# Kernel optimization log

Hardware: AMD Instinct MI355X
Metric: run time of the kernel (lower is better)

Reference implementation:

```python
import jax, jax.numpy as jnp
import numpy as np

EPS = 1e-5  # torch BatchNorm1d default

def _silu(x):
    return x * jax.nn.sigmoid(x)

def _bn(x, g, b, rm, rv, axis):
    # eval-mode batchnorm along given channel axis
    shape = [1] * x.ndim
    shape[axis] = -1
    return (x - rm.reshape(shape)) * (g.reshape(shape) / jnp.sqrt(rv.reshape(shape) + EPS)) + b.reshape(shape)

def setup_inputs() -> dict:
    key = jax.random.key(0)
    ks = jax.random.split(key, 12)
    b, n, p, d, r = 64, 256, 12, 128, 2
    x = jax.random.normal(ks[0], (b, n, p, d), dtype=jnp.float32)
    # k branch: Conv1d(p -> 1, k=1, bias=False) + BN(1)
    wk = jax.random.normal(ks[1], (p,), dtype=jnp.float32) / np.sqrt(p)
    bn_k_g = jax.random.uniform(ks[2], (1,), dtype=jnp.float32, minval=0.5, maxval=1.5)
    bn_k_b = 0.1 * jax.random.normal(ks[3], (1,), dtype=jnp.float32)
    bn_k_rm = jnp.zeros((1,), jnp.float32)
    bn_k_rv = jnp.ones((1,), jnp.float32)
    # v branch: Conv1d(d -> d, k=1, bias=False) + BN(d)
    wv = jax.random.normal(ks[4], (d, d), dtype=jnp.float32) / np.sqrt(d)
    bn_v_g = jax.random.uniform(ks[5], (d,), dtype=jnp.float32, minval=0.5, maxval=1.5)
    bn_v_b = 0.1 * jax.random.normal(ks[6], (d,), dtype=jnp.float32)
    bn_v_rm = jnp.zeros((d,), jnp.float32)
    bn_v_rv = jnp.ones((d,), jnp.float32)
    # fc_avg / fc_max: Linear(n, n//r, bias=False) -> GELU -> Linear(n//r, n, bias=False)
    w_avg1 = jax.random.normal(ks[7], (n // r, n), dtype=jnp.float32) / np.sqrt(n)
    w_avg2 = jax.random.normal(ks[8], (n, n // r), dtype=jnp.float32) / np.sqrt(n // r)
    w_max1 = jax.random.normal(ks[9], (n // r, n), dtype=jnp.float32) / np.sqrt(n)
    w_max2 = jax.random.normal(ks[10], (n, n // r), dtype=jnp.float32) / np.sqrt(n // r)
    return dict(x=x, wk=wk, bn_k_g=bn_k_g, bn_k_b=bn_k_b, bn_k_rm=bn_k_rm, bn_k_rv=bn_k_rv,
                wv=wv, bn_v_g=bn_v_g, bn_v_b=bn_v_b, bn_v_rm=bn_v_rm, bn_v_rv=bn_v_rv,
                w_avg1=w_avg1, w_avg2=w_avg2, w_max1=w_max1, w_max2=w_max2)

def _forward(x, wk, bn_k_g, bn_k_b, bn_k_rm, bn_k_rv, wv, bn_v_g, bn_v_b, bn_v_rm, bn_v_rv,
             w_avg1, w_avg2, w_max1, w_max2):
    b, n, p, d = x.shape
    xf = x.reshape(b * n, p, d)
    # squeeze-excite gates: pool over d, FC over n
    avg = jnp.mean(xf, axis=-1).reshape(b, n, p).transpose(0, 2, 1)  # [b,p,n]
    mx = jnp.max(xf, axis=-1).reshape(b, n, p).transpose(0, 2, 1)    # [b,p,n]
    gelu = lambda t: jax.nn.gelu(t, approximate=False)
    avg_g = jax.nn.sigmoid(gelu(avg @ w_avg1.T) @ w_avg2.T).transpose(0, 2, 1)  # [b,n,p]
    max_g = jax.nn.sigmoid(gelu(mx @ w_max1.T) @ w_max2.T).transpose(0, 2, 1)   # [b,n,p]
    # k: 1x1 conv over p channels -> [bn, d], BN(1ch), SiLU, softmax over d
    k_raw = jnp.einsum('bpd,p->bd', xf, wk)
    k = jax.nn.softmax(_silu(k_raw * (bn_k_g / jnp.sqrt(bn_k_rv + EPS)) - bn_k_rm * (bn_k_g / jnp.sqrt(bn_k_rv + EPS)) + bn_k_b), axis=-1)  # [bn,d]
    # v: 1x1 conv over d channels on [bn,d,p], BN(d), SiLU -> [bn,p,d]
    v_raw = jnp.einsum('bpd,ed->bpe', xf, wv)  # channel axis is last here
    v = _silu(_bn(v_raw, bn_v_g, bn_v_b, bn_v_rm, bn_v_rv, axis=2))  # [bn,p,d]
    # y = v @ k : [bn,p];  y_pool = (max+avg) @ v : [bn,d]
    y = jnp.einsum('bpd,bd->bp', v, k)
    pool = (max_g + avg_g).reshape(b * n, p)
    y_pool = jnp.einsum('bp,bpd->bd', pool, v)
    out = y_pool[:, None, :] * y[:, :, None]  # [bn,p,d]
    return out.reshape(b, n, p, d)

def reference(x, wk, bn_k_g, bn_k_b, bn_k_rm, bn_k_rv, wv, bn_v_g, bn_v_b, bn_v_rm, bn_v_rv,
              w_avg1, w_avg2, w_max1, w_max2):
    return _forward(x, wk, bn_k_g, bn_k_b, bn_k_rm, bn_k_rv, wv, bn_v_g, bn_v_b, bn_v_rm, bn_v_rv,
                    w_avg1, w_avg2, w_max1, w_max2)
```

## Files before the change

kernel.cpp:

```cpp
#include <hip/hip_runtime.h>
#include <hip/hip_bf16.h>

#define B_   64
#define N_   256
#define P_   12
#define D_   128
#define BN_  (B_*N_)
#define EPSV 1e-5f

typedef float  f32x4  __attribute__((ext_vector_type(4)));
typedef __bf16 bf16x8 __attribute__((ext_vector_type(8)));
typedef __bf16 bf16x4 __attribute__((ext_vector_type(4)));

__device__ float g_avg[768*256];
__device__ float g_mx [768*256];
__device__ float g_h1 [1536*128];
__device__ float g_pool[BN_*P_];

__device__ inline float sigm_(float x) { return 1.0f / (1.0f + __expf(-x)); }

__device__ inline float dot4_(float4 a, float4 b, float acc) {
  acc = fmaf(a.x, b.x, acc); acc = fmaf(a.y, b.y, acc);
  acc = fmaf(a.z, b.z, acc); acc = fmaf(a.w, b.w, acc);
  return acc;
}

__global__ __launch_bounds__(256) void k1_pool(const float* __restrict__ x) {
  int w = threadIdx.x >> 6, l = threadIdx.x & 63;
  int bn = blockIdx.x * 4 + w;
  const float* xp = x + (size_t)bn * (P_ * D_);
  int b = bn >> 8, n = bn & 255;
  float sacc[P_], macc[P_];
#pragma unroll
  for (int p = 0; p < P_; ++p) {
    float2 v = *(const float2*)(xp + p * D_ + 2 * l);
    float s = v.x + v.y;
    float m = fmaxf(v.x, v.y);
#pragma unroll
    for (int off = 32; off; off >>= 1) {
      s += __shfl_xor(s, off);
      m = fmaxf(m, __shfl_xor(m, off));
    }
    sacc[p] = s * (1.0f / D_);
    macc[p] = m;
  }
  if (l == 0) {
#pragma unroll
    for (int p = 0; p < P_; ++p) {
      g_avg[(b * P_ + p) * N_ + n] = sacc[p];
      g_mx [(b * P_ + p) * N_ + n] = macc[p];
    }
  }
}

__global__ __launch_bounds__(256) void k2_l1(const float* __restrict__ w_avg1,
                                             const float* __restrict__ w_max1) {
  __shared__ float in_t[16 * 256];
  __shared__ float w_t[64 * 68];
  int t = threadIdx.x;
  int rblk = blockIdx.x % 96, cblk = blockIdx.x / 96;
  int rr0 = rblk * 16, c0 = cblk * 64;
  bool mxb = (rr0 >= 768);
  int r768 = mxb ? rr0 - 768 : rr0;
  const float* in = (mxb ? g_mx : g_avg) + (size_t)r768 * 256;
  const float* w1 = mxb ? w_max1 : w_avg1;
#pragma unroll
  for (int i = 0; i < 4; ++i) {
    int F = t + i * 256, r = F >> 6, k4 = F & 63;
    *(float4*)(in_t + r * 256 + k4 * 4) = *(const float4*)(in + r * 256 + k4 * 4);
  }
  int c = t & 63, rq = t >> 6;
  float a0 = 0, a1 = 0, a2 = 0, a3 = 0;
  for (int kc = 0; kc < 4; ++kc) {
    __syncthreads();
#pragma unroll
    for (int i = 0; i < 4; ++i) {
      int F = t + i * 256, cr = F >> 4, k4 = F & 15;
      *(float4*)(w_t + cr * 68 + k4 * 4) =
          *(const float4*)(w1 + (size_t)(c0 + cr) * 256 + kc * 64 + k4 * 4);
    }
    __syncthreads();
#pragma unroll
    for (int k4 = 0; k4 < 16; ++k4) {
      float4 wv4 = *(float4*)(w_t + c * 68 + k4 * 4);
      a0 = dot4_(*(float4*)(in_t + (rq * 4 + 0) * 256 + kc * 64 + k4 * 4), wv4, a0);
      a1 = dot4_(*(float4*)(in_t + (rq * 4 + 1) * 256 + kc * 64 + k4 * 4), wv4, a1);
      a2 = dot4_(*(float4*)(in_t + (rq * 4 + 2) * 256 + kc * 64 + k4 * 4), wv4, a2);
      a3 = dot4_(*(float4*)(in_t + (rq * 4 + 3) * 256 + kc * 64 + k4 * 4), wv4, a3);
    }
  }
  float accs[4] = {a0, a1, a2, a3};
#pragma unroll
  for (int r = 0; r < 4; ++r) {
    float a = accs[r];
    float g = 0.5f * a * (1.0f + erff(a * 0.70710678f));
    g_h1[(size_t)(rr0 + rq * 4 + r) * 128 + c0 + c] = g;
  }
}

__global__ __launch_bounds__(256) void k2_l2(const float* __restrict__ w_avg2,
                                             const float* __restrict__ w_max2) {
  __shared__ float ina_t[16 * 128];
  __shared__ float inm_t[16 * 128];
  __shared__ float wa_t[64 * 68];
  __shared__ float wm_t[64 * 68];
  int t = threadIdx.x;
  int rblk = blockIdx.x % 48, cblk = blockIdx.x / 48;
  int rr0 = rblk * 16, n0 = cblk * 64;
#pragma unroll
  for (int i = 0; i < 2; ++i) {
    int F = t + i * 256, r = F >> 5, k4 = F & 31;
    *(float4*)(ina_t + r * 128 + k4 * 4) = *(const float4*)(g_h1 + (size_t)(rr0 + r) * 128 + k4 * 4);
    *(float4*)(inm_t + r * 128 + k4 * 4) = *(const float4*)(g_h1 + (size_t)(768 + rr0 + r) * 128 + k4 * 4);
  }
  int c = t & 63, rq = t >> 6;
  float aa0=0, aa1=0, aa2=0, aa3=0, am0=0, am1=0, am2=0, am3=0;
  for (int kc = 0; kc < 2; ++kc) {
    __syncthreads();
#pragma unroll
    for (int i = 0; i < 4; ++i) {
      int F = t + i * 256, cr = F >> 4, k4 = F & 15;
      *(float4*)(wa_t + cr * 68 + k4 * 4) =
          *(const float4*)(w_avg2 + (size_t)(n0 + cr) * 128 + kc * 64 + k4 * 4);
      *(float4*)(wm_t + cr * 68 + k4 * 4) =
          *(const float4*)(w_max2 + (size_t)(n0 + cr) * 128 + kc * 64 + k4 * 4);
    }
    __syncthreads();
#pragma unroll
    for (int k4 = 0; k4 < 16; ++k4) {
      float4 wa4 = *(float4*)(wa_t + c * 68 + k4 * 4);
      float4 wm4 = *(float4*)(wm_t + c * 68 + k4 * 4);
      float4 i0 = *(float4*)(ina_t + (rq * 4 + 0) * 128 + kc * 64 + k4 * 4);
      float4 i1 = *(float4*)(ina_t + (rq * 4 + 1) * 128 + kc * 64 + k4 * 4);
      float4 i2 = *(float4*)(ina_t + (rq * 4 + 2) * 128 + kc * 64 + k4 * 4);
      float4 i3 = *(float4*)(ina_t + (rq * 4 + 3) * 128 + kc * 64 + k4 * 4);
      aa0 = dot4_(i0, wa4, aa0); aa1 = dot4_(i1, wa4, aa1);
      aa2 = dot4_(i2, wa4, aa2); aa3 = dot4_(i3, wa4, aa3);
      float4 j0 = *(float4*)(inm_t + (rq * 4 + 0) * 128 + kc * 64 + k4 * 4);
      float4 j1 = *(float4*)(inm_t + (rq * 4 + 1) * 128 + kc * 64 + k4 * 4);
      float4 j2 = *(float4*)(inm_t + (rq * 4 + 2) * 128 + kc * 64 + k4 * 4);
      float4 j3 = *(float4*)(inm_t + (rq * 4 + 3) * 128 + kc * 64 + k4 * 4);
      am0 = dot4_(j0, wm4, am0); am1 = dot4_(j1, wm4, am1);
      am2 = dot4_(j2, wm4, am2); am3 = dot4_(j3, wm4, am3);
    }
  }
  float va[4] = {aa0, aa1, aa2, aa3};
  float vm[4] = {am0, am1, am2, am3};
#pragma unroll
  for (int r = 0; r < 4; ++r) {
    int rr = rr0 + rq * 4 + r;
    int b = rr / 12, p = rr % 12;
    float pv = sigm_(va[r]) + sigm_(vm[r]);
    g_pool[((size_t)b * 256 + (n0 + c)) * 12 + p] = pv;
  }
}

__global__ __launch_bounds__(256) void k3_main(
    const float* __restrict__ x,  const float* __restrict__ wk,
    const float* __restrict__ kg, const float* __restrict__ kb,
    const float* __restrict__ krm, const float* __restrict__ krv,
    const float* __restrict__ wv,
    const float* __restrict__ vg, const float* __restrict__ vb,
    const float* __restrict__ vrm, const float* __restrict__ vrv,
    float* __restrict__ out) {
  __shared__ __align__(16) __bf16 wv_lds[128 * 128];
  __shared__ float sv_l[128], tv_l[128];
  __shared__ float v_l[4][12 * 128];

  int t = threadIdx.x, w = t >> 6, l = t & 63;
  if (t < 128) {
    float s = vg[t] * rsqrtf(vrv[t] + EPSV);
    sv_l[t] = s;
    tv_l[t] = vb[t] - vrm[t] * s;
  }
  __syncthreads();
  {
    int e = t >> 1, dh = (t & 1) * 64;
    float s = sv_l[e];
    int swz = (e & 7) << 4;
#pragma unroll
    for (int i = 0; i < 16; ++i) {
      float4 v4 = *(const float4*)(wv + (size_t)e * 128 + dh + i * 4);
      bf16x4 h;
      h[0] = (__bf16)(v4.x * s); h[1] = (__bf16)(v4.y * s);
      h[2] = (__bf16)(v4.z * s); h[3] = (__bf16)(v4.w * s);
      int byte = (e * 256 + (dh + i * 4) * 2) ^ swz;
      *(bf16x4*)((char*)wv_lds + byte) = h;
    }
  }
  float ksc = kg[0] * rsqrtf(krv[0] + EPSV);
  float kbs = kb[0] - krm[0] * ksc;
  __syncthreads();

  int arow = (l & 15) > 11 ? 11 : (l & 15);
  int ak = (l >> 4) * 8;
  int bcol = l & 15;
  int bko = (l >> 4) * 16;

  for (int it = 0; it < 4; ++it) {
    int bn = blockIdx.x * 16 + it * 4 + w;
    const float* xp = x + (size_t)bn * (P_ * D_);

    bf16x8 afr[4];
#pragma unroll
    for (int ks = 0; ks < 4; ++ks) {
      const float* src = xp + arow * 128 + ks * 32 + ak;
      float4 lo = *(const float4*)(src);
      float4 hi = *(const float4*)(src + 4);
      bf16x8 a;
      a[0] = (__bf16)lo.x; a[1] = (__bf16)lo.y; a[2] = (__bf16)lo.z; a[3] = (__bf16)lo.w;
      a[4] = (__bf16)hi.x; a[5] = (__bf16)hi.y; a[6] = (__bf16)hi.z; a[7] = (__bf16)hi.w;
      afr[ks] = a;
    }

    float kr0 = 0, kr1 = 0;
#pragma unroll
    for (int p = 0; p < P_; ++p) {
      float2 xv = *(const float2*)(xp + p * 128 + 2 * l);
      float wkp = wk[p];
      kr0 = fmaf(xv.x, wkp, kr0);
      kr1 = fmaf(xv.y, wkp, kr1);
    }
    float z0 = kr0 * ksc + kbs, z1 = kr1 * ksc + kbs;
    z0 = z0 * sigm_(z0);
    z1 = z1 * sigm_(z1);
    float mmax = fmaxf(z0, z1);
#pragma unroll
    for (int off = 32; off; off >>= 1) mmax = fmaxf(mmax, __shfl_xor(mmax, off));
    float e0 = __expf(z0 - mmax), e1 = __expf(z1 - mmax);
    float es = e0 + e1;
#pragma unroll
    for (int off = 32; off; off >>= 1) es += __shfl_xor(es, off);
    float inv = 1.0f / es;
    float k0 = e0 * inv, k1 = e1 * inv;

    f32x4 acc[8];
#pragma unroll
    for (int nt = 0; nt < 8; ++nt) acc[nt] = (f32x4){0.f, 0.f, 0.f, 0.f};
#pragma unroll
    for (int nt = 0; nt < 8; ++nt) {
      int er = bcol + nt * 16;
      int base = er * 256;
      int sw = (er & 7) << 4;
#pragma unroll
      for (int ks = 0; ks < 4; ++ks) {
        int byte = (base + ks * 64 + bko) ^ sw;
        bf16x8 bfr = *(const bf16x8*)((const char*)wv_lds + byte);
        acc[nt] = __builtin_amdgcn_mfma_f32_16x16x32_bf16(afr[ks], bfr, acc[nt], 0, 0, 0);
      }
    }

    int p0 = (l >> 4) * 4;
    if (p0 < 12) {
#pragma unroll
      for (int nt = 0; nt < 8; ++nt) {
        int e = bcol + nt * 16;
        float tvv = tv_l[e];
#pragma unroll
        for (int r = 0; r < 4; ++r) {
          float a = acc[nt][r] + tvv;
          float v = a * sigm_(a);
          v_l[w][(p0 + r) * 128 + e] = v;
        }
      }
    }
    __syncthreads();

    const float* pp = g_pool + (size_t)bn * 12;
    float pl[P_];
#pragma unroll
    for (int p = 0; p < P_; ++p) pl[p] = pp[p];
    float yp0 = 0, yp1 = 0;
    float ypart[P_];
#pragma unroll
    for (int p = 0; p < P_; ++p) {
      float2 vvp = *(const float2*)(&v_l[w][0] + p * 128 + 2 * l);
      ypart[p] = vvp.x * k0 + vvp.y * k1;
      yp0 = fmaf(pl[p], vvp.x, yp0);
      yp1 = fmaf(pl[p], vvp.y, yp1);
    }
#pragma unroll
    for (int p = 0; p < P_; ++p) {
      float s = ypart[p];
#pragma unroll
      for (int off = 32; off; off >>= 1) s += __shfl_xor(s, off);
      ypart[p] = s;
    }
    float* op = out + (size_t)bn * (P_ * D_);
#pragma unroll
    for (int p = 0; p < P_; ++p) {
      float2 o;
      o.x = yp0 * ypart[p];
      o.y = yp1 * ypart[p];
      *(float2*)(op + p * 128 + 2 * l) = o;
    }
    __syncthreads();
  }
}

extern "C" void kernel_launch(void* const* d_in, const int* in_sizes, int n_in,
                              void* d_out, int out_size, void* d_ws, size_t ws_size,
                              hipStream_t stream) {
  const float* x   = (const float*)d_in[0];
  const float* wk  = (const float*)d_in[1];
  const float* kg  = (const float*)d_in[2];
  const float* kbb = (const float*)d_in[3];
  const float* krm = (const float*)d_in[4];
  const float* krv = (const float*)d_in[5];
  const float* wvp = (const float*)d_in[6];
  const float* vg  = (const float*)d_in[7];
  const float* vbb = (const float*)d_in[8];
  const float* vrm = (const float*)d_in[9];
  const float* vrv = (const float*)d_in[10];
  const float* wa1 = (const float*)d_in[11];
  const float* wa2 = (const float*)d_in[12];
  const float* wm1 = (const float*)d_in[13];
  const float* wm2 = (const float*)d_in[14];
  float* out = (float*)d_out;

  k1_pool<<<4096, 256, 0, stream>>>(x);
  k2_l1<<<192, 256, 0, stream>>>(wa1, wm1);
  k2_l2<<<192, 256, 0, stream>>>(wa2, wm2);
  k3_main<<<1024, 256, 0, stream>>>(x, wk, kg, kbb, krm, krv, wvp, vg, vbb, vrm, vrv, out);
}
```

Before: 123.1 us.

## Drop block barriers in main loop, pad V tile, widen pool loads

Each wavefront in the main kernel works on its own private v_l slice, so the two __syncthreads per iteration are removed and the wave relies on in-wave ordering instead. The v_l row stride is padded to 130 floats to cut LDS bank conflicts, and the g_pool gate loads are moved ahead of the MFMA section so their latency overlaps compute. The pooling kernel now uses float4 loads with two p rows per wave (32-lane reductions). Removing the barriers assumes LDS writes and reads within one wavefront are ordered without an explicit wave barrier, which is a correctness risk.

```diff
diff --git a/kernel.cpp b/kernel.cpp
--- a/kernel.cpp
+++ b/kernel.cpp
@@ -7,6 +7,7 @@
 #define D_   128
 #define BN_  (B_*N_)
 #define EPSV 1e-5f
+#define VST  130
 
 typedef float  f32x4  __attribute__((ext_vector_type(4)));
 typedef __bf16 bf16x8 __attribute__((ext_vector_type(8)));
@@ -29,26 +30,29 @@
   int w = threadIdx.x >> 6, l = threadIdx.x & 63;
   int bn = blockIdx.x * 4 + w;
   const float* xp = x + (size_t)bn * (P_ * D_);
-  int b = bn >> 8, n = bn & 255;
-  float sacc[P_], macc[P_];
-#pragma unroll
-  for (int p = 0; p < P_; ++p) {
-    float2 v = *(const float2*)(xp + p * D_ + 2 * l);
-    float s = v.x + v.y;
-    float m = fmaxf(v.x, v.y);
-#pragma unroll
-    for (int off = 32; off; off >>= 1) {
+  int half = l >> 5, lane32 = l & 31;
+  float s6[6], m6[6];
+#pragma unroll
+  for (int pp = 0; pp < 6; ++pp) {
+    int p = pp * 2 + half;
+    float4 v = *(const float4*)(xp + p * D_ + lane32 * 4);
+    float s = (v.x + v.y) + (v.z + v.w);
+    float m = fmaxf(fmaxf(v.x, v.y), fmaxf(v.z, v.w));
+#pragma unroll
+    for (int off = 16; off; off >>= 1) {
       s += __shfl_xor(s, off);
       m = fmaxf(m, __shfl_xor(m, off));
     }
-    sacc[p] = s * (1.0f / D_);
-    macc[p] = m;
-  }
-  if (l == 0) {
-#pragma unroll
-    for (int p = 0; p < P_; ++p) {
-      g_avg[(b * P_ + p) * N_ + n] = sacc[p];
-      g_mx [(b * P_ + p) * N_ + n] = macc[p];
+    s6[pp] = s * (1.0f / D_);
+    m6[pp] = m;
+  }
+  if (lane32 == 0) {
+    int b = bn >> 8, n = bn & 255;
+#pragma unroll
+    for (int pp = 0; pp < 6; ++pp) {
+      int p = pp * 2 + half;
+      g_avg[(b * P_ + p) * N_ + n] = s6[pp];
+      g_mx [(b * P_ + p) * N_ + n] = m6[pp];
     }
   }
 }
@@ -165,7 +169,7 @@
     float* __restrict__ out) {
   __shared__ __align__(16) __bf16 wv_lds[128 * 128];
   __shared__ float sv_l[128], tv_l[128];
-  __shared__ float v_l[4][12 * 128];
+  __shared__ float v_l[4][P_ * VST];
 
   int t = threadIdx.x, w = t >> 6, l = t & 63;
   if (t < 128) {
@@ -196,10 +200,16 @@
   int ak = (l >> 4) * 8;
   int bcol = l & 15;
   int bko = (l >> 4) * 16;
+  float* vw = &v_l[w][0];
 
   for (int it = 0; it < 4; ++it) {
     int bn = blockIdx.x * 16 + it * 4 + w;
     const float* xp = x + (size_t)bn * (P_ * D_);
+
+    const float* pp = g_pool + (size_t)bn * 12;
+    float pl[P_];
+#pragma unroll
+    for (int p = 0; p < P_; ++p) pl[p] = pp[p];
 
     bf16x8 afr[4];
 #pragma unroll
@@ -260,21 +270,16 @@
         for (int r = 0; r < 4; ++r) {
           float a = acc[nt][r] + tvv;
           float v = a * sigm_(a);
-          v_l[w][(p0 + r) * 128 + e] = v;
+          vw[(p0 + r) * VST + e] = v;
         }
       }
     }
-    __syncthreads();
-
-    const float* pp = g_pool + (size_t)bn * 12;
-    float pl[P_];
-#pragma unroll
-    for (int p = 0; p < P_; ++p) pl[p] = pp[p];
+
     float yp0 = 0, yp1 = 0;
     float ypart[P_];
 #pragma unroll
     for (int p = 0; p < P_; ++p) {
-      float2 vvp = *(const float2*)(&v_l[w][0] + p * 128 + 2 * l);
+      float2 vvp = *(const float2*)(vw + p * VST + 2 * l);
       ypart[p] = vvp.x * k0 + vvp.y * k1;
       yp0 = fmaf(pl[p], vvp.x, yp0);
       yp1 = fmaf(pl[p], vvp.y, yp1);
@@ -294,7 +299,6 @@
       o.y = yp1 * ypart[p];
       *(float2*)(op + p * 128 + 2 * l) = o;
     }
-    __syncthreads();
   }
 }
 
```

After: 107.8 us. -12.4%, faster.
